# Kernel optimization log

Measured on AMD Instinct MI355X. Metric: run time of the kernel, lower is better.

Reference implementation:

```python
import jax, jax.numpy as jnp
import numpy as np

N_NODES = 15000
N_EDGES = 60000
NODE_VOCAB = 118 + 20000
EDGE_VOCAB = 4 + 50
NODE_INDIM = 64
EDGE_INDIM = 32
H = 32          # node_hidden_feats
EH = 64         # edge_hidden_feats
NUM_STEPS = 3   # num_step_message_passing
N_BOND_TYPES = 4  # edge ids < 4 are chemical bonds -> edge_func1, else knowledge relations -> edge_func2


def setup_inputs() -> dict:
    key = jax.random.key(0)
    ks = jax.random.split(key, 20)
    s = 0.05  # param scale for numerical stability
    return {
        "node_ids": jax.random.randint(ks[0], (N_NODES,), 0, NODE_VOCAB),
        "edge_ids": jax.random.randint(ks[1], (N_EDGES,), 0, EDGE_VOCAB),
        "src": jax.random.randint(ks[2], (N_EDGES,), 0, N_NODES),
        "dst": jax.random.randint(ks[3], (N_EDGES,), 0, N_NODES),
        "node_table": jax.random.normal(ks[4], (NODE_VOCAB, NODE_INDIM), jnp.float32),
        "edge_table": jax.random.normal(ks[5], (EDGE_VOCAB, EDGE_INDIM), jnp.float32),
        "proj_W": jax.random.normal(ks[6], (H, NODE_INDIM), jnp.float32) * s,
        "proj_b": jnp.zeros((H,), jnp.float32),
        "attn_w": jax.random.normal(ks[7], (2 * H,), jnp.float32) * s,
        "e1_W1": jax.random.normal(ks[8], (EH, EDGE_INDIM), jnp.float32) * s,
        "e1_b1": jnp.zeros((EH,), jnp.float32),
        "e1_W2": jax.random.normal(ks[9], (H * H, EH), jnp.float32) * s,
        "e1_b2": jnp.zeros((H * H,), jnp.float32),
        "e2_W1": jax.random.normal(ks[10], (EH, EDGE_INDIM), jnp.float32) * s,
        "e2_b1": jnp.zeros((EH,), jnp.float32),
        "e2_W2": jax.random.normal(ks[11], (H * H, EH), jnp.float32) * s,
        "e2_b2": jnp.zeros((H * H,), jnp.float32),
        "gru_Wih": jax.random.normal(ks[12], (3 * H, H), jnp.float32) * s,
        "gru_Whh": jax.random.normal(ks[13], (3 * H, H), jnp.float32) * s,
        "gru_bih": jnp.zeros((3 * H,), jnp.float32),
        "gru_bhh": jnp.zeros((3 * H,), jnp.float32),
    }


def _edge_softmax(logits, dst, num_nodes):
    # softmax over incoming edges of each destination node
    m = jax.ops.segment_max(logits, dst, num_segments=num_nodes)
    ex = jnp.exp(logits - m[dst])
    s = jax.ops.segment_sum(ex, dst, num_segments=num_nodes)
    return ex / s[dst]


def reference(node_ids, edge_ids, src, dst, node_table, edge_table, proj_W, proj_b,
              attn_w, e1_W1, e1_b1, e1_W2, e1_b2, e2_W1, e2_b1, e2_W2, e2_b2,
              gru_Wih, gru_Whh, gru_bih, gru_bhh):
    # --- embedding lookups ---
    nf = node_table[node_ids]                      # [N, node_indim]
    ef = edge_table[edge_ids]                      # [E, edge_indim]
    # --- project node feats: Linear + ReLU ---
    h = jax.nn.relu(nf @ proj_W.T + proj_b)        # [N, H]

    # --- per-edge weight matrices from the two edge MLPs (edge feats are
    # constant across message-passing steps, so compute once) ---
    def edge_mlp(W1, b1, W2, b2):
        z = jax.nn.relu(ef @ W1.T + b1)            # [E, EH]
        return (z @ W2.T + b2).reshape(-1, H, H)   # [E, H, H]

    W_e1 = edge_mlp(e1_W1, e1_b1, e1_W2, e1_b2)
    W_e2 = edge_mlp(e2_W1, e2_b1, e2_W2, e2_b2)
    is_bond = (edge_ids < N_BOND_TYPES)[:, None, None]
    W_edge = jnp.where(is_bond, W_e1, W_e2)        # [E, H, H]

    hidden = h                                     # GRU hidden state (seq of len 1 -> GRUCell)
    for _ in range(NUM_STEPS):
        # attention logits on edges: leaky_relu(attn_fc([h_src || h_dst]))
        a = jax.nn.leaky_relu(
            h[src] @ attn_w[:H] + h[dst] @ attn_w[H:])     # [E]
        alpha = _edge_softmax(a, dst, N_NODES)             # [E]
        # edge-conditioned message: (h_src @ W_e) weighted by attention
        msg = jnp.einsum('ei,eio->eo', h[src], W_edge) * alpha[:, None]  # [E, H]
        agg = jax.ops.segment_sum(msg, dst, num_segments=N_NODES)       # [N, H]
        m = jax.nn.relu(agg)
        # single GRU step (torch nn.GRU, 1 layer, seq_len 1)
        gi = m @ gru_Wih.T + gru_bih               # [N, 3H]
        gh = hidden @ gru_Whh.T + gru_bhh          # [N, 3H]
        ir, iz, inn = jnp.split(gi, 3, axis=1)
        hr, hz, hn = jnp.split(gh, 3, axis=1)
        r = jax.nn.sigmoid(ir + hr)
        z = jax.nn.sigmoid(iz + hz)
        n = jnp.tanh(inn + r * hn)
        hidden = (1.0 - z) * n + z * hidden
        h = hidden
    return h
```

## Files before the change

### kernel.cpp

```cpp
#include <hip/hip_runtime.h>
#include <hip/hip_bf16.h>
#include <math.h>

#define N_NODES   15000
#define N_EDGES   60000
#define EVOCAB    54
#define NODE_INDIM 64
#define EDGE_INDIM 32
#define H  32
#define EH 64
#define N_BOND 4

#define TASK_VOCAB (EVOCAB * 1024)
#define TASK_PROJ  (N_NODES * H)
#define TASK_ZERO  ((N_NODES * H + N_NODES) / 4)
#define TASK_PACK  (3 * H * H)
#define TA (TASK_VOCAB + TASK_PROJ + TASK_ZERO + TASK_PACK)

__global__ void setup_kernel(const int* __restrict__ node_ids,
                             const float* __restrict__ node_table,
                             const float* __restrict__ edge_table,
                             const float* __restrict__ proj_W, const float* __restrict__ proj_b,
                             const float* __restrict__ e1_W1, const float* __restrict__ e1_b1,
                             const float* __restrict__ e1_W2, const float* __restrict__ e1_b2,
                             const float* __restrict__ e2_W1, const float* __restrict__ e2_b1,
                             const float* __restrict__ e2_W2, const float* __restrict__ e2_b2,
                             const float* __restrict__ gWih, const float* __restrict__ gWhh,
                             float* __restrict__ Wt, float* __restrict__ h,
                             float* __restrict__ agg,
                             float4* __restrict__ Wpk4, float2* __restrict__ Wpk2) {
    int t = blockIdx.x * 256 + threadIdx.x;
    if (t >= TA) return;
    if (t < TASK_VOCAB) {
        int v = t >> 10, f = t & 1023, l = t & 63;
        const float* W1 = (v < N_BOND) ? e1_W1 : e2_W1;
        const float* b1 = (v < N_BOND) ? e1_b1 : e2_b1;
        const float* W2 = (v < N_BOND) ? e1_W2 : e2_W2;
        const float* b2 = (v < N_BOND) ? e1_b2 : e2_b2;
        const float* ef = edge_table + v * EDGE_INDIM;
        float z = b1[l];
        const float* w1r = W1 + l * EDGE_INDIM;
        #pragma unroll
        for (int j = 0; j < EDGE_INDIM; ++j) z += ef[j] * w1r[j];
        z = fmaxf(z, 0.f);
        float y = b2[f];
        const float* w2r = W2 + f * EH;
        #pragma unroll
        for (int k = 0; k < EH; ++k) y += __shfl(z, k, 64) * w2r[k];
        Wt[v * 1024 + f] = y;
    } else if (t < TASK_VOCAB + TASK_PROJ) {
        int q = t - TASK_VOCAB;
        int n = q >> 5, o = q & 31;
        int gid = node_ids[n];
        const float* nf = node_table + (size_t)gid * NODE_INDIM;
        const float* wr = proj_W + o * NODE_INDIM;
        float acc = proj_b[o];
        #pragma unroll 8
        for (int j = 0; j < NODE_INDIM; ++j) acc += nf[j] * wr[j];
        h[q] = fmaxf(acc, 0.f);
    } else if (t < TASK_VOCAB + TASK_PROJ + TASK_ZERO) {
        int q = t - TASK_VOCAB - TASK_PROJ;
        ((float4*)agg)[q] = make_float4(0.f, 0.f, 0.f, 0.f);
    } else {
        int q = t - TASK_VOCAB - TASK_PROJ - TASK_ZERO;
        int j = q >> 5, o = q & 31;
        Wpk4[q] = make_float4(gWih[o * 32 + j], gWih[(32 + o) * 32 + j],
                              gWih[(64 + o) * 32 + j], gWhh[o * 32 + j]);
        Wpk2[q] = make_float2(gWhh[(32 + o) * 32 + j], gWhh[(64 + o) * 32 + j]);
    }
}

__launch_bounds__(256)
__global__ void edge_kernel(const int* __restrict__ src, const int* __restrict__ dst,
                            const int* __restrict__ edge_ids,
                            const float* __restrict__ h, const float* __restrict__ Wt,
                            const float* __restrict__ attn_w,
                            float* __restrict__ agg, float* __restrict__ sm) {
    int t = blockIdx.x * 256 + threadIdx.x;
    int e = t >> 5, o = t & 31;
    int s = src[e], d = dst[e], v = edge_ids[e];
    float hs = h[s * 32 + o];
    float val = hs * attn_w[o] + h[d * 32 + o] * attn_w[32 + o];
    #pragma unroll
    for (int k = 16; k > 0; k >>= 1) val += __shfl_xor(val, k, 32);
    float a  = (val > 0.f) ? val : 0.01f * val;
    float ex = __expf(a);
    const float* W = Wt + v * 1024 + o;
    float y = 0.f;
    #pragma unroll
    for (int i = 0; i < 32; ++i)
        y += __shfl(hs, i, 32) * W[i * 32];
    atomicAdd(&agg[d * 32 + o], ex * y);
    if (o == 0) atomicAdd(&sm[d], ex);
}

__launch_bounds__(256)
__global__ void gru_kernel(float* __restrict__ agg, float* __restrict__ sm,
                           const float* __restrict__ h,
                           const float4* __restrict__ Wpk4, const float2* __restrict__ Wpk2,
                           const float* __restrict__ gbih, const float* __restrict__ gbhh,
                           float* __restrict__ hout) {
    int t = blockIdx.x * 256 + threadIdx.x;
    int n = t >> 5, o = t & 31;
    float sinv = 1.f / sm[n];
    float m  = fmaxf(agg[t] * sinv, 0.f);
    float hv = h[t];
    float gir = 0.f, giz = 0.f, gin = 0.f, ghr = 0.f, ghz = 0.f, ghn = 0.f;
    #pragma unroll 8
    for (int j = 0; j < 32; ++j) {
        float mj = __shfl(m, j, 32);
        float hj = __shfl(hv, j, 32);
        float4 a = Wpk4[j * 32 + o];
        float2 b = Wpk2[j * 32 + o];
        gir += mj * a.x;  giz += mj * a.y;  gin += mj * a.z;
        ghr += hj * a.w;  ghz += hj * b.x;  ghn += hj * b.y;
    }
    float r  = 1.f / (1.f + __expf(-(gir + gbih[o]      + ghr + gbhh[o])));
    float z  = 1.f / (1.f + __expf(-(giz + gbih[32 + o] + ghz + gbhh[32 + o])));
    float nn = tanhf(gin + gbih[64 + o] + r * (ghn + gbhh[64 + o]));
    hout[t] = (1.f - z) * nn + z * hv;
    agg[t] = 0.f;
    if (o == 0) sm[n] = 0.f;
}

extern "C" void kernel_launch(void* const* d_in, const int* in_sizes, int n_in,
                              void* d_out, int out_size, void* d_ws, size_t ws_size,
                              hipStream_t stream) {
    const int*   node_ids   = (const int*)d_in[0];
    const int*   edge_ids   = (const int*)d_in[1];
    const int*   src        = (const int*)d_in[2];
    const int*   dst        = (const int*)d_in[3];
    const float* node_table = (const float*)d_in[4];
    const float* edge_table = (const float*)d_in[5];
    const float* proj_W     = (const float*)d_in[6];
    const float* proj_b     = (const float*)d_in[7];
    const float* attn_w     = (const float*)d_in[8];
    const float* e1_W1 = (const float*)d_in[9];  const float* e1_b1 = (const float*)d_in[10];
    const float* e1_W2 = (const float*)d_in[11]; const float* e1_b2 = (const float*)d_in[12];
    const float* e2_W1 = (const float*)d_in[13]; const float* e2_b1 = (const float*)d_in[14];
    const float* e2_W2 = (const float*)d_in[15]; const float* e2_b2 = (const float*)d_in[16];
    const float* gWih  = (const float*)d_in[17]; const float* gWhh  = (const float*)d_in[18];
    const float* gbih  = (const float*)d_in[19]; const float* gbhh  = (const float*)d_in[20];

    char* ws = (char*)d_ws;
    float*  Wt   = (float*)(ws);
    float*  h    = (float*)(ws + 221184);
    float*  agg  = (float*)(ws + 221184 + 1920000);
    float*  sm   = (float*)(ws + 221184 + 3840000);
    float4* Wpk4 = (float4*)(ws + 221184 + 3840000 + 60000);
    float2* Wpk2 = (float2*)(ws + 221184 + 3840000 + 60000 + 49152);
    float*  out  = (float*)d_out;

    setup_kernel<<<(TA + 255) / 256, 256, 0, stream>>>(
        node_ids, node_table, edge_table, proj_W, proj_b,
        e1_W1, e1_b1, e1_W2, e1_b2, e2_W1, e2_b1, e2_W2, e2_b2,
        gWih, gWhh, Wt, h, agg, Wpk4, Wpk2);

    for (int step = 0; step < 3; ++step) {
        edge_kernel<<<(N_EDGES * 32) / 256, 256, 0, stream>>>(
            src, dst, edge_ids, h, Wt, attn_w, agg, sm);
        float* hout = (step == 2) ? out : h;
        gru_kernel<<<(N_NODES * 32) / 256, 256, 0, stream>>>(
            agg, sm, h, Wpk4, Wpk2, gbih, gbhh, hout);
    }
}
```

Before: 226.3 us.

## Build CSR by destination and fuse edge aggregation with GRU per node

Builds a destination-sorted CSR once (histogram, single-block scan, scatter), then replaces the atomic edge kernel plus GRU kernel with one pull-style step kernel per iteration that gathers incoming edges per node, accumulates the softmax numerator and denominator in registers, and applies the GRU directly. This removes the float atomics, the agg/sm buffers and their zeroing, and halves the launches per step. Setup loads are also vectorised to float4. In exchange it adds three preprocessing launches, including a serial single-block scan, and per-node loops whose length varies with degree, which can cause wave divergence and load imbalance.

```diff
diff --git a/kernel.cpp b/kernel.cpp
--- a/kernel.cpp
+++ b/kernel.cpp
@@ -13,9 +13,9 @@
 
 #define TASK_VOCAB (EVOCAB * 1024)
 #define TASK_PROJ  (N_NODES * H)
-#define TASK_ZERO  ((N_NODES * H + N_NODES) / 4)
 #define TASK_PACK  (3 * H * H)
-#define TA (TASK_VOCAB + TASK_PROJ + TASK_ZERO + TASK_PACK)
+#define TASK_ZDEG  (N_NODES)
+#define TA (TASK_VOCAB + TASK_PROJ + TASK_PACK + TASK_ZDEG)
 
 __global__ void setup_kernel(const int* __restrict__ node_ids,
                              const float* __restrict__ node_table,
@@ -27,8 +27,8 @@
                              const float* __restrict__ e2_W2, const float* __restrict__ e2_b2,
                              const float* __restrict__ gWih, const float* __restrict__ gWhh,
                              float* __restrict__ Wt, float* __restrict__ h,
-                             float* __restrict__ agg,
-                             float4* __restrict__ Wpk4, float2* __restrict__ Wpk2) {
+                             float4* __restrict__ Wpk4, float2* __restrict__ Wpk2,
+                             int* __restrict__ deg) {
     int t = blockIdx.x * 256 + threadIdx.x;
     if (t >= TA) return;
     if (t < TASK_VOCAB) {
@@ -37,90 +37,127 @@
         const float* b1 = (v < N_BOND) ? e1_b1 : e2_b1;
         const float* W2 = (v < N_BOND) ? e1_W2 : e2_W2;
         const float* b2 = (v < N_BOND) ? e1_b2 : e2_b2;
-        const float* ef = edge_table + v * EDGE_INDIM;
+        const float4* ef4 = (const float4*)(edge_table + v * EDGE_INDIM);
+        const float4* w1r = (const float4*)(W1 + l * EDGE_INDIM);
         float z = b1[l];
-        const float* w1r = W1 + l * EDGE_INDIM;
-        #pragma unroll
-        for (int j = 0; j < EDGE_INDIM; ++j) z += ef[j] * w1r[j];
+        #pragma unroll
+        for (int c = 0; c < 8; ++c) {
+            float4 e4 = ef4[c], w4 = w1r[c];
+            z += e4.x * w4.x + e4.y * w4.y + e4.z * w4.z + e4.w * w4.w;
+        }
         z = fmaxf(z, 0.f);
+        const float4* w2r = (const float4*)(W2 + f * EH);
         float y = b2[f];
-        const float* w2r = W2 + f * EH;
-        #pragma unroll
-        for (int k = 0; k < EH; ++k) y += __shfl(z, k, 64) * w2r[k];
+        #pragma unroll
+        for (int c = 0; c < 16; ++c) {
+            float4 w4 = w2r[c];
+            y += __shfl(z, 4 * c,     64) * w4.x;
+            y += __shfl(z, 4 * c + 1, 64) * w4.y;
+            y += __shfl(z, 4 * c + 2, 64) * w4.z;
+            y += __shfl(z, 4 * c + 3, 64) * w4.w;
+        }
         Wt[v * 1024 + f] = y;
     } else if (t < TASK_VOCAB + TASK_PROJ) {
         int q = t - TASK_VOCAB;
         int n = q >> 5, o = q & 31;
         int gid = node_ids[n];
-        const float* nf = node_table + (size_t)gid * NODE_INDIM;
-        const float* wr = proj_W + o * NODE_INDIM;
+        const float4* nf4 = (const float4*)(node_table + (size_t)gid * NODE_INDIM);
+        const float4* wr4 = (const float4*)(proj_W + o * NODE_INDIM);
         float acc = proj_b[o];
-        #pragma unroll 8
-        for (int j = 0; j < NODE_INDIM; ++j) acc += nf[j] * wr[j];
+        #pragma unroll
+        for (int c = 0; c < 16; ++c) {
+            float4 a = nf4[c], w = wr4[c];
+            acc += a.x * w.x + a.y * w.y + a.z * w.z + a.w * w.w;
+        }
         h[q] = fmaxf(acc, 0.f);
-    } else if (t < TASK_VOCAB + TASK_PROJ + TASK_ZERO) {
+    } else if (t < TASK_VOCAB + TASK_PROJ + TASK_PACK) {
         int q = t - TASK_VOCAB - TASK_PROJ;
-        ((float4*)agg)[q] = make_float4(0.f, 0.f, 0.f, 0.f);
-    } else {
-        int q = t - TASK_VOCAB - TASK_PROJ - TASK_ZERO;
         int j = q >> 5, o = q & 31;
         Wpk4[q] = make_float4(gWih[o * 32 + j], gWih[(32 + o) * 32 + j],
                               gWih[(64 + o) * 32 + j], gWhh[o * 32 + j]);
         Wpk2[q] = make_float2(gWhh[(32 + o) * 32 + j], gWhh[(64 + o) * 32 + j]);
-    }
+    } else {
+        deg[t - TASK_VOCAB - TASK_PROJ - TASK_PACK] = 0;
+    }
+}
+
+__global__ void hist_kernel(const int* __restrict__ dst, int* __restrict__ deg,
+                            int* __restrict__ rank) {
+    int e = blockIdx.x * 256 + threadIdx.x;
+    if (e < N_EDGES) rank[e] = atomicAdd(&deg[dst[e]], 1);
+}
+
+__global__ void scan_kernel(const int* __restrict__ deg, int* __restrict__ off) {
+    __shared__ int lsum[256];
+    int t = threadIdx.x;
+    int beg = t * 59, end = min(beg + 59, N_NODES);
+    int s = 0;
+    for (int i = beg; i < end; ++i) s += deg[i];
+    lsum[t] = s;
+    __syncthreads();
+    for (int d2 = 1; d2 < 256; d2 <<= 1) {
+        int v = (t >= d2) ? lsum[t - d2] : 0;
+        __syncthreads();
+        lsum[t] += v;
+        __syncthreads();
+    }
+    int run = lsum[t] - s;
+    if (t == 0) off[0] = 0;
+    for (int i = beg; i < end; ++i) { run += deg[i]; off[i + 1] = run; }
+}
+
+__global__ void scatter_kernel(const int* __restrict__ dst, const int* __restrict__ off,
+                               const int* __restrict__ rank, int* __restrict__ csr) {
+    int e = blockIdx.x * 256 + threadIdx.x;
+    if (e < N_EDGES) csr[off[dst[e]] + rank[e]] = e;
 }
 
 __launch_bounds__(256)
-__global__ void edge_kernel(const int* __restrict__ src, const int* __restrict__ dst,
-                            const int* __restrict__ edge_ids,
-                            const float* __restrict__ h, const float* __restrict__ Wt,
-                            const float* __restrict__ attn_w,
-                            float* __restrict__ agg, float* __restrict__ sm) {
-    int t = blockIdx.x * 256 + threadIdx.x;
-    int e = t >> 5, o = t & 31;
-    int s = src[e], d = dst[e], v = edge_ids[e];
-    float hs = h[s * 32 + o];
-    float val = hs * attn_w[o] + h[d * 32 + o] * attn_w[32 + o];
-    #pragma unroll
-    for (int k = 16; k > 0; k >>= 1) val += __shfl_xor(val, k, 32);
-    float a  = (val > 0.f) ? val : 0.01f * val;
-    float ex = __expf(a);
-    const float* W = Wt + v * 1024 + o;
-    float y = 0.f;
-    #pragma unroll
-    for (int i = 0; i < 32; ++i)
-        y += __shfl(hs, i, 32) * W[i * 32];
-    atomicAdd(&agg[d * 32 + o], ex * y);
-    if (o == 0) atomicAdd(&sm[d], ex);
-}
-
-__launch_bounds__(256)
-__global__ void gru_kernel(float* __restrict__ agg, float* __restrict__ sm,
-                           const float* __restrict__ h,
-                           const float4* __restrict__ Wpk4, const float2* __restrict__ Wpk2,
-                           const float* __restrict__ gbih, const float* __restrict__ gbhh,
-                           float* __restrict__ hout) {
+__global__ void step_kernel(const float* __restrict__ hcur,
+                            const int* __restrict__ off, const int* __restrict__ csr,
+                            const int* __restrict__ src, const int* __restrict__ edge_ids,
+                            const float* __restrict__ Wt, const float* __restrict__ attn_w,
+                            const float4* __restrict__ Wpk4, const float2* __restrict__ Wpk2,
+                            const float* __restrict__ gbih, const float* __restrict__ gbhh,
+                            float* __restrict__ hout) {
     int t = blockIdx.x * 256 + threadIdx.x;
     int n = t >> 5, o = t & 31;
-    float sinv = 1.f / sm[n];
-    float m  = fmaxf(agg[t] * sinv, 0.f);
-    float hv = h[t];
+    float hd  = hcur[n * 32 + o];
+    float aw0 = attn_w[o], aw1 = attn_w[32 + o];
+    float num = 0.f, den = 0.f;
+    int k1 = off[n + 1];
+    for (int k = off[n]; k < k1; ++k) {
+        int e = csr[k];
+        int s = src[e], v = edge_ids[e];
+        float hs = hcur[s * 32 + o];
+        float val = hs * aw0 + hd * aw1;
+        #pragma unroll
+        for (int m = 16; m > 0; m >>= 1) val += __shfl_xor(val, m, 32);
+        float a  = (val > 0.f) ? val : 0.01f * val;
+        float ex = __expf(a);
+        const float* W = Wt + v * 1024 + o;
+        float y = 0.f;
+        #pragma unroll
+        for (int i = 0; i < 32; ++i)
+            y += __shfl(hs, i, 32) * W[i * 32];
+        num += ex * y;
+        den += ex;
+    }
+    float m = (den > 0.f) ? fmaxf(num / den, 0.f) : 0.f;
     float gir = 0.f, giz = 0.f, gin = 0.f, ghr = 0.f, ghz = 0.f, ghn = 0.f;
     #pragma unroll 8
     for (int j = 0; j < 32; ++j) {
-        float mj = __shfl(m, j, 32);
-        float hj = __shfl(hv, j, 32);
-        float4 a = Wpk4[j * 32 + o];
-        float2 b = Wpk2[j * 32 + o];
-        gir += mj * a.x;  giz += mj * a.y;  gin += mj * a.z;
-        ghr += hj * a.w;  ghz += hj * b.x;  ghn += hj * b.y;
+        float mj = __shfl(m,  j, 32);
+        float hj = __shfl(hd, j, 32);
+        float4 a4 = Wpk4[j * 32 + o];
+        float2 b2 = Wpk2[j * 32 + o];
+        gir += mj * a4.x;  giz += mj * a4.y;  gin += mj * a4.z;
+        ghr += hj * a4.w;  ghz += hj * b2.x;  ghn += hj * b2.y;
     }
     float r  = 1.f / (1.f + __expf(-(gir + gbih[o]      + ghr + gbhh[o])));
     float z  = 1.f / (1.f + __expf(-(giz + gbih[32 + o] + ghz + gbhh[32 + o])));
     float nn = tanhf(gin + gbih[64 + o] + r * (ghn + gbhh[64 + o]));
-    hout[t] = (1.f - z) * nn + z * hv;
-    agg[t] = 0.f;
-    if (o == 0) sm[n] = 0.f;
+    hout[t] = (1.f - z) * nn + z * hd;
 }
 
 extern "C" void kernel_launch(void* const* d_in, const int* in_sizes, int n_in,
@@ -144,23 +181,28 @@
 
     char* ws = (char*)d_ws;
     float*  Wt   = (float*)(ws);
-    float*  h    = (float*)(ws + 221184);
-    float*  agg  = (float*)(ws + 221184 + 1920000);
-    float*  sm   = (float*)(ws + 221184 + 3840000);
-    float4* Wpk4 = (float4*)(ws + 221184 + 3840000 + 60000);
-    float2* Wpk2 = (float2*)(ws + 221184 + 3840000 + 60000 + 49152);
+    float*  h_a  = (float*)(ws + 221184);
+    float*  h_b  = (float*)(ws + 2141184);
+    float4* Wpk4 = (float4*)(ws + 4061184);
+    float2* Wpk2 = (float2*)(ws + 4110336);
+    int*    deg  = (int*)(ws + 4134912);
+    int*    off  = (int*)(ws + 4194912);
+    int*    rank = (int*)(ws + 4254916);
+    int*    csr  = (int*)(ws + 4494916);
     float*  out  = (float*)d_out;
 
     setup_kernel<<<(TA + 255) / 256, 256, 0, stream>>>(
         node_ids, node_table, edge_table, proj_W, proj_b,
         e1_W1, e1_b1, e1_W2, e1_b2, e2_W1, e2_b1, e2_W2, e2_b2,
-        gWih, gWhh, Wt, h, agg, Wpk4, Wpk2);
-
-    for (int step = 0; step < 3; ++step) {
-        edge_kernel<<<(N_EDGES * 32) / 256, 256, 0, stream>>>(
-            src, dst, edge_ids, h, Wt, attn_w, agg, sm);
-        float* hout = (step == 2) ? out : h;
-        gru_kernel<<<(N_NODES * 32) / 256, 256, 0, stream>>>(
-            agg, sm, h, Wpk4, Wpk2, gbih, gbhh, hout);
-    }
-}
+        gWih, gWhh, Wt, h_a, Wpk4, Wpk2, deg);
+    hist_kernel<<<(N_EDGES + 255) / 256, 256, 0, stream>>>(dst, deg, rank);
+    scan_kernel<<<1, 256, 0, stream>>>(deg, off);
+    scatter_kernel<<<(N_EDGES + 255) / 256, 256, 0, stream>>>(dst, off, rank, csr);
+
+    step_kernel<<<1875, 256, 0, stream>>>(h_a, off, csr, src, edge_ids, Wt, attn_w,
+                                          Wpk4, Wpk2, gbih, gbhh, h_b);
+    step_kernel<<<1875, 256, 0, stream>>>(h_b, off, csr, src, edge_ids, Wt, attn_w,
+                                          Wpk4, Wpk2, gbih, gbhh, h_a);
+    step_kernel<<<1875, 256, 0, stream>>>(h_a, off, csr, src, edge_ids, Wt, attn_w,
+                                          Wpk4, Wpk2, gbih, gbhh, out);
+}
```

Result: slower. 274.5 us (+21.3%).
